# Kernel tuning notes

Measured on AMD Instinct MI355X. Metric: run time of the kernel, lower is better.

Reference implementation:

```python
import jax, jax.numpy as jnp
import numpy as np

N, E, H = 50000, 800000, 4

def setup_inputs() -> dict:
    key = jax.random.key(0)
    ks = jax.random.split(key, 16)
    feat = jax.random.normal(ks[0], (N, 2), dtype=jnp.float32)
    src = jax.random.randint(ks[1], (E,), 0, N, dtype=jnp.int32)
    dst = jax.random.randint(ks[2], (E,), 0, N, dtype=jnp.int32)
    def w(k, shape, fan_in):
        return jax.random.normal(k, shape, dtype=jnp.float32) * (1.0 / np.sqrt(fan_in))
    # layer 1: 2 -> 4 heads x 32
    W1 = w(ks[3], (2, 128), 2); al1 = w(ks[4], (H, 32), 32); ar1 = w(ks[5], (H, 32), 32); b1 = jnp.zeros((128,), jnp.float32)
    # layer 2: 128 -> 4 heads x 32
    W2 = w(ks[6], (128, 128), 128); al2 = w(ks[7], (H, 32), 32); ar2 = w(ks[8], (H, 32), 32); b2 = jnp.zeros((128,), jnp.float32)
    # layer 3: 128 -> 4 heads x 64
    W3 = w(ks[9], (128, 256), 128); al3 = w(ks[10], (H, 64), 64); ar3 = w(ks[11], (H, 64), 64); b3 = jnp.zeros((256,), jnp.float32)
    return dict(feat=feat, src=src, dst=dst, W1=W1, al1=al1, ar1=ar1, b1=b1,
                W2=W2, al2=al2, ar2=ar2, b2=b2, W3=W3, al3=al3, ar3=ar3, b3=b3)

def gat_layer(h, W, al, ar, b, src, dst):
    # h: [N, Fin]; W: [Fin, H*D]; al/ar: [H, D]; b: [H*D]
    Hh, D = al.shape
    z = (h @ W).reshape(-1, Hh, D)                      # [N, H, D]
    el = jnp.sum(z * al[None], axis=-1)                 # [N, H]
    er = jnp.sum(z * ar[None], axis=-1)                 # [N, H]
    e = jax.nn.leaky_relu(el[src] + er[dst], 0.2)       # [E, H]
    m = jax.ops.segment_max(e, dst, num_segments=N)     # [N, H] per-dst max
    ex = jnp.exp(e - m[dst])                            # [E, H]
    s = jax.ops.segment_sum(ex, dst, num_segments=N)    # [N, H]
    alpha = ex / s[dst]                                 # edge softmax
    msg = z[src] * alpha[:, :, None]                    # [E, H, D] gathered+weighted
    out = jax.ops.segment_sum(msg, dst, num_segments=N) # [N, H, D]
    return out.reshape(N, Hh * D) + b

def reference(feat, src, dst, W1, al1, ar1, b1, W2, al2, ar2, b2, W3, al3, ar3, b3):
    # dropout is identity at inference
    h = jax.nn.relu(gat_layer(feat, W1, al1, ar1, b1, src, dst))
    h = jax.nn.relu(gat_layer(h, W2, al2, ar2, b2, src, dst))
    h = gat_layer(h, W3, al3, ar3, b3, src, dst)
    return h
```

## Files before the change

### kernel.cpp

```cpp
#include <hip/hip_runtime.h>
#include <math.h>


#define NEG_BIG (-1e38f)

typedef _Float16 h8 __attribute__((ext_vector_type(8)));
typedef _Float16 h4 __attribute__((ext_vector_type(4)));

static inline int cdiv(int a, int b) { return (a + b - 1) / b; }

__device__ __forceinline__ float lrelu(float x) { return (x >= 0.f) ? x : 0.2f * x; }


__global__ void count_deg_kernel(const int* __restrict__ dst, int* __restrict__ deg, int E) {
    int i = blockIdx.x * blockDim.x + threadIdx.x;
    if (i < E) atomicAdd(&deg[dst[i]], 1);
}

__global__ __launch_bounds__(256) void scan1_kernel(const int* __restrict__ deg,
                                                    int* __restrict__ rowptr,
                                                    int* __restrict__ bsum, int n) {
    __shared__ int wsum[4];
    int t = threadIdx.x;
    int l = t & 63, wv = t >> 6;
    int i = blockIdx.x * 256 + t;
    int v = (i < n) ? deg[i] : 0;
    int x = v;
    #pragma unroll
    for (int off = 1; off < 64; off <<= 1) {
        int y = __shfl_up(x, off);
        if (l >= off) x += y;
    }
    if (l == 63) wsum[wv] = x;
    __syncthreads();
    int wo = 0;
    #pragma unroll
    for (int j = 0; j < 4; ++j)
        if (j < wv) wo += wsum[j];
    if (i < n) rowptr[i] = wo + x - v;
    if (t == 255) bsum[blockIdx.x] = wo + x;
}

__global__ __launch_bounds__(256) void scan2_kernel(const int* __restrict__ bsum,
                                                    int* __restrict__ boff, int nb) {
    __shared__ int wsum[4];
    int t = threadIdx.x;
    int l = t & 63, wv = t >> 6;
    int v = (t < nb) ? bsum[t] : 0;
    int x = v;
    #pragma unroll
    for (int off = 1; off < 64; off <<= 1) {
        int y = __shfl_up(x, off);
        if (l >= off) x += y;
    }
    if (l == 63) wsum[wv] = x;
    __syncthreads();
    int wo = 0;
    #pragma unroll
    for (int j = 0; j < 4; ++j)
        if (j < wv) wo += wsum[j];
    if (t < nb) boff[t] = wo + x - v;
}

__global__ __launch_bounds__(256) void scan3_kernel(int* __restrict__ rowptr,
                                                    const int* __restrict__ boff,
                                                    int n, int E) {
    int i = blockIdx.x * 256 + threadIdx.x;
    if (i < n) rowptr[i] += boff[blockIdx.x];
    if (i == 0) rowptr[n] = E;
}

__global__ void fill_csr_kernel(const int* __restrict__ src, const int* __restrict__ dst,
                                const int* __restrict__ rowptr,
                                int* __restrict__ cursor, int* __restrict__ csrc, int E) {
    int i = blockIdx.x * blockDim.x + threadIdx.x;
    if (i < E) {
        int d = dst[i];
        int pos = atomicAdd(&cursor[d], 1);
        csrc[rowptr[d] + pos] = src[i];
    }
}


__global__ void z1_kernel(const float* __restrict__ feat, const float* __restrict__ W1,
                          const float* __restrict__ al, const float* __restrict__ ar,
                          _Float16* __restrict__ zh, float* __restrict__ el,
                          float* __restrict__ er, int N) {
    int l = threadIdx.x & 63;
    int v = blockIdx.x * 4 + (threadIdx.x >> 6);
    if (v >= N) return;
    float f0 = feat[(size_t)v * 2];
    float f1 = feat[(size_t)v * 2 + 1];
    float z0 = fmaf(f0, W1[l], f1 * W1[128 + l]);
    float z1v = fmaf(f0, W1[l + 64], f1 * W1[128 + l + 64]);
    zh[(size_t)v * 128 + l] = (_Float16)z0;
    zh[(size_t)v * 128 + l + 64] = (_Float16)z1v;
    float pl0 = z0 * al[l], pl1 = z1v * al[l + 64];
    float pr0 = z0 * ar[l], pr1 = z1v * ar[l + 64];
    #pragma unroll
    for (int off = 1; off < 32; off <<= 1) {
        pl0 += __shfl_xor(pl0, off);
        pl1 += __shfl_xor(pl1, off);
        pr0 += __shfl_xor(pr0, off);
        pr1 += __shfl_xor(pr1, off);
    }
    if ((l & 31) == 0) {
        int g = l >> 5;
        el[(size_t)v * 4 + g] = pl0;
        el[(size_t)v * 4 + 2 + g] = pl1;
        er[(size_t)v * 4 + g] = pr0;
        er[(size_t)v * 4 + 2 + g] = pr1;
    }
}


template <int HDOUT>
__global__ __launch_bounds__(256) void gemm_tile_kernel(
        const _Float16* __restrict__ A, const float* __restrict__ W,
        const float* __restrict__ al, const float* __restrict__ ar,
        _Float16* __restrict__ ZH, float* __restrict__ el, float* __restrict__ er,
        int N) {
    __shared__ __align__(16) float AT[64][132];
    __shared__ __align__(16) float WS[64][64];
    int n0 = blockIdx.x * 128;
    int c0 = blockIdx.y * 64;
    int t = threadIdx.x;
    int tr = t >> 4;
    int tc = t & 15;

    float acc[8][4] = {};

    for (int kc = 0; kc < 128; kc += 64) {
        {
            int kk = (t & 7) * 8;
            int rb = t >> 3;
            #pragma unroll
            for (int it = 0; it < 4; ++it) {
                int r = rb + 32 * it;
                int n = n0 + r;
                h8 a;
                #pragma unroll
                for (int j = 0; j < 8; ++j) a[j] = (_Float16)0.f;
                if (n < N) a = *(const h8*)&A[(size_t)n * 128 + kc + kk];
                #pragma unroll
                for (int j = 0; j < 8; ++j) AT[kk + j][r] = (float)a[j];
            }
        }
        {
            int cc = (t & 15) * 4;
            int kb = t >> 4;
            #pragma unroll
            for (int it = 0; it < 4; ++it) {
                int k = kb + 16 * it;
                *(float4*)&WS[k][cc] =
                    *(const float4*)&W[(size_t)(kc + k) * HDOUT + c0 + cc];
            }
        }
        __syncthreads();

        #pragma unroll 4
        for (int k = 0; k < 64; ++k) {
            float4 a0 = *(const float4*)&AT[k][tr * 8];
            float4 a1 = *(const float4*)&AT[k][tr * 8 + 4];
            float4 wv = *(const float4*)&WS[k][tc * 4];
            acc[0][0] = fmaf(a0.x, wv.x, acc[0][0]); acc[0][1] = fmaf(a0.x, wv.y, acc[0][1]);
            acc[0][2] = fmaf(a0.x, wv.z, acc[0][2]); acc[0][3] = fmaf(a0.x, wv.w, acc[0][3]);
            acc[1][0] = fmaf(a0.y, wv.x, acc[1][0]); acc[1][1] = fmaf(a0.y, wv.y, acc[1][1]);
            acc[1][2] = fmaf(a0.y, wv.z, acc[1][2]); acc[1][3] = fmaf(a0.y, wv.w, acc[1][3]);
            acc[2][0] = fmaf(a0.z, wv.x, acc[2][0]); acc[2][1] = fmaf(a0.z, wv.y, acc[2][1]);
            acc[2][2] = fmaf(a0.z, wv.z, acc[2][2]); acc[2][3] = fmaf(a0.z, wv.w, acc[2][3]);
            acc[3][0] = fmaf(a0.w, wv.x, acc[3][0]); acc[3][1] = fmaf(a0.w, wv.y, acc[3][1]);
            acc[3][2] = fmaf(a0.w, wv.z, acc[3][2]); acc[3][3] = fmaf(a0.w, wv.w, acc[3][3]);
            acc[4][0] = fmaf(a1.x, wv.x, acc[4][0]); acc[4][1] = fmaf(a1.x, wv.y, acc[4][1]);
            acc[4][2] = fmaf(a1.x, wv.z, acc[4][2]); acc[4][3] = fmaf(a1.x, wv.w, acc[4][3]);
            acc[5][0] = fmaf(a1.y, wv.x, acc[5][0]); acc[5][1] = fmaf(a1.y, wv.y, acc[5][1]);
            acc[5][2] = fmaf(a1.y, wv.z, acc[5][2]); acc[5][3] = fmaf(a1.y, wv.w, acc[5][3]);
            acc[6][0] = fmaf(a1.z, wv.x, acc[6][0]); acc[6][1] = fmaf(a1.z, wv.y, acc[6][1]);
            acc[6][2] = fmaf(a1.z, wv.z, acc[6][2]); acc[6][3] = fmaf(a1.z, wv.w, acc[6][3]);
            acc[7][0] = fmaf(a1.w, wv.x, acc[7][0]); acc[7][1] = fmaf(a1.w, wv.y, acc[7][1]);
            acc[7][2] = fmaf(a1.w, wv.z, acc[7][2]); acc[7][3] = fmaf(a1.w, wv.w, acc[7][3]);
        }
        __syncthreads();
    }

    float4 alv = *(const float4*)&al[c0 + tc * 4];
    float4 arv = *(const float4*)&ar[c0 + tc * 4];

    #pragma unroll
    for (int i = 0; i < 8; ++i) {
        int n = n0 + tr * 8 + i;
        bool ok = (n < N);
        if (ok) {
            h4 hz4 = { (_Float16)acc[i][0], (_Float16)acc[i][1],
                       (_Float16)acc[i][2], (_Float16)acc[i][3] };
            *(h4*)&ZH[(size_t)n * HDOUT + c0 + tc * 4] = hz4;
        }
        float pe = acc[i][0] * alv.x + acc[i][1] * alv.y +
                   acc[i][2] * alv.z + acc[i][3] * alv.w;
        float pr = acc[i][0] * arv.x + acc[i][1] * arv.y +
                   acc[i][2] * arv.z + acc[i][3] * arv.w;
        if (HDOUT == 128) {
            #pragma unroll
            for (int off = 1; off < 8; off <<= 1) {
                pe += __shfl_xor(pe, off);
                pr += __shfl_xor(pr, off);
            }
            if (ok && (tc & 7) == 0) {
                int h = 2 * blockIdx.y + (tc >> 3);
                el[(size_t)n * 4 + h] = pe;
                er[(size_t)n * 4 + h] = pr;
            }
        } else {
            #pragma unroll
            for (int off = 1; off < 16; off <<= 1) {
                pe += __shfl_xor(pe, off);
                pr += __shfl_xor(pr, off);
            }
            if (ok && tc == 0) {
                int h = blockIdx.y;
                el[(size_t)n * 4 + h] = pe;
                er[(size_t)n * 4 + h] = pr;
            }
        }
    }
}


template <bool RELU, int GRP, int HD, typename OUTT>
__global__ __launch_bounds__(256) void agg_kernel(
        const _Float16* __restrict__ zh, const float* __restrict__ el,
        const float* __restrict__ er, const int* __restrict__ rowptr,
        const int* __restrict__ csrc, const float* __restrict__ bias,
        OUTT* __restrict__ out, int N) {
    constexpr int NV = 64 / GRP;
    constexpr int CH = HD / GRP;
    constexpr int HGRP = GRP / 4;
    static_assert(CH == 8, "config assumes 8 channels per lane");
    __shared__ float exs[4][NV][4][GRP + 1];
    __shared__ int   svs[4][NV][GRP + 1];
    const int l = threadIdx.x & 63;
    const int w = threadIdx.x >> 6;
    const int g = l / GRP;
    const int lg = l & (GRP - 1);
    const int v = blockIdx.x * (4 * NV) + w * NV + g;
    if (v >= N) return;
    const int r0 = rowptr[v], r1 = rowptr[v + 1];
    const int c0 = lg * CH;
    const int h = lg / HGRP;
    float4 b0 = *(const float4*)(bias + c0);
    float4 b1 = *(const float4*)(bias + c0 + 4);
    float4 o0, o1;

    if (r0 == r1) {
        o0 = b0; o1 = b1;
    } else {
        float4 er4 = *(const float4*)(er + (size_t)v * 4);

        float m0 = NEG_BIG, m1 = NEG_BIG, m2 = NEG_BIG, m3 = NEG_BIG;
        int sv0 = 0;
        float4 e40 = make_float4(NEG_BIG, NEG_BIG, NEG_BIG, NEG_BIG);
        for (int base = r0; base < r1; base += GRP) {
            int i = base + lg;
            float ex_ = NEG_BIG, ey_ = NEG_BIG, ez_ = NEG_BIG, ew_ = NEG_BIG;
            int sv = 0;
            if (i < r1) {
                sv = csrc[i];
                float4 ev = *(const float4*)(el + (size_t)sv * 4);
                ex_ = lrelu(ev.x + er4.x);
                ey_ = lrelu(ev.y + er4.y);
                ez_ = lrelu(ev.z + er4.z);
                ew_ = lrelu(ev.w + er4.w);
            }
            if (base == r0) { sv0 = sv; e40 = make_float4(ex_, ey_, ez_, ew_); }
            m0 = fmaxf(m0, ex_); m1 = fmaxf(m1, ey_);
            m2 = fmaxf(m2, ez_); m3 = fmaxf(m3, ew_);
        }
        #pragma unroll
        for (int off = 1; off < GRP; off <<= 1) {
            m0 = fmaxf(m0, __shfl_xor(m0, off));
            m1 = fmaxf(m1, __shfl_xor(m1, off));
            m2 = fmaxf(m2, __shfl_xor(m2, off));
            m3 = fmaxf(m3, __shfl_xor(m3, off));
        }

        float s0 = 0.f, s1 = 0.f, s2 = 0.f, s3 = 0.f;
        float4 a0 = make_float4(0.f, 0.f, 0.f, 0.f);
        float4 a1 = make_float4(0.f, 0.f, 0.f, 0.f);

        for (int base = r0; base < r1; base += GRP) {
            int i = base + lg;
            int sv; float4 e4;
            if (base == r0) {
                sv = sv0; e4 = e40;
            } else if (i < r1) {
                sv = csrc[i];
                float4 ev = *(const float4*)(el + (size_t)sv * 4);
                e4 = make_float4(lrelu(ev.x + er4.x), lrelu(ev.y + er4.y),
                                 lrelu(ev.z + er4.z), lrelu(ev.w + er4.w));
            } else {
                sv = 0; e4 = make_float4(NEG_BIG, NEG_BIG, NEG_BIG, NEG_BIG);
            }
            bool valid = (i < r1);
            float exv0 = valid ? __expf(e4.x - m0) : 0.f;
            float exv1 = valid ? __expf(e4.y - m1) : 0.f;
            float exv2 = valid ? __expf(e4.z - m2) : 0.f;
            float exv3 = valid ? __expf(e4.w - m3) : 0.f;
            s0 += exv0; s1 += exv1; s2 += exv2; s3 += exv3;
            svs[w][g][lg] = sv;
            exs[w][g][0][lg] = exv0; exs[w][g][1][lg] = exv1;
            exs[w][g][2][lg] = exv2; exs[w][g][3][lg] = exv3;
            int cnt = min(GRP, r1 - base);
            #pragma unroll 8
            for (int k = 0; k < cnt; ++k) {
                int svk = svs[w][g][k];
                float exk = exs[w][g][h][k];
                h8 zz = *(const h8*)(zh + (size_t)svk * HD + c0);
                a0.x = fmaf((float)zz[0], exk, a0.x);
                a0.y = fmaf((float)zz[1], exk, a0.y);
                a0.z = fmaf((float)zz[2], exk, a0.z);
                a0.w = fmaf((float)zz[3], exk, a0.w);
                a1.x = fmaf((float)zz[4], exk, a1.x);
                a1.y = fmaf((float)zz[5], exk, a1.y);
                a1.z = fmaf((float)zz[6], exk, a1.z);
                a1.w = fmaf((float)zz[7], exk, a1.w);
            }
        }
        #pragma unroll
        for (int off = 1; off < GRP; off <<= 1) {
            s0 += __shfl_xor(s0, off);
            s1 += __shfl_xor(s1, off);
            s2 += __shfl_xor(s2, off);
            s3 += __shfl_xor(s3, off);
        }
        float s = (h == 0) ? s0 : (h == 1) ? s1 : (h == 2) ? s2 : s3;
        float inv = 1.f / s;
        o0 = make_float4(fmaf(a0.x, inv, b0.x), fmaf(a0.y, inv, b0.y),
                         fmaf(a0.z, inv, b0.z), fmaf(a0.w, inv, b0.w));
        o1 = make_float4(fmaf(a1.x, inv, b1.x), fmaf(a1.y, inv, b1.y),
                         fmaf(a1.z, inv, b1.z), fmaf(a1.w, inv, b1.w));
    }
    if (RELU) {
        o0.x = fmaxf(o0.x, 0.f); o0.y = fmaxf(o0.y, 0.f);
        o0.z = fmaxf(o0.z, 0.f); o0.w = fmaxf(o0.w, 0.f);
        o1.x = fmaxf(o1.x, 0.f); o1.y = fmaxf(o1.y, 0.f);
        o1.z = fmaxf(o1.z, 0.f); o1.w = fmaxf(o1.w, 0.f);
    }
    if constexpr (sizeof(OUTT) == 2) {
        h8 ho;
        ho[0] = (_Float16)o0.x; ho[1] = (_Float16)o0.y;
        ho[2] = (_Float16)o0.z; ho[3] = (_Float16)o0.w;
        ho[4] = (_Float16)o1.x; ho[5] = (_Float16)o1.y;
        ho[6] = (_Float16)o1.z; ho[7] = (_Float16)o1.w;
        *(h8*)((_Float16*)out + (size_t)v * HD + c0) = ho;
    } else {
        float* op = (float*)out + (size_t)v * HD + c0;
        *(float4*)op = o0;
        *(float4*)(op + 4) = o1;
    }
}


extern "C" void kernel_launch(void* const* d_in, const int* in_sizes, int n_in,
                              void* d_out, int out_size, void* d_ws, size_t ws_size,
                              hipStream_t stream) {
    const float* feat = (const float*)d_in[0];
    const int* src = (const int*)d_in[1];
    const int* dst = (const int*)d_in[2];
    const float* W1 = (const float*)d_in[3];
    const float* al1 = (const float*)d_in[4];
    const float* ar1 = (const float*)d_in[5];
    const float* b1 = (const float*)d_in[6];
    const float* W2 = (const float*)d_in[7];
    const float* al2 = (const float*)d_in[8];
    const float* ar2 = (const float*)d_in[9];
    const float* b2 = (const float*)d_in[10];
    const float* W3 = (const float*)d_in[11];
    const float* al3 = (const float*)d_in[12];
    const float* ar3 = (const float*)d_in[13];
    const float* b3 = (const float*)d_in[14];
    const int N = in_sizes[0] / 2;
    const int E = in_sizes[1];

    _Float16* hbuf = (_Float16*)d_ws;
    float* el = (float*)(hbuf + (size_t)N * 128);
    float* er = el + (size_t)N * 4;
    _Float16* zh = (_Float16*)(er + (size_t)N * 4);
    int* csrc = (int*)(zh + (size_t)N * 256);
    int* deg = csrc + E;
    int* cursor = deg + N;
    int* rowptr = cursor + N;
    int* bsum = rowptr + (N + 1);
    int* boff = bsum + 256;

    const int nb = cdiv(N, 256);

    hipMemsetAsync(deg, 0, sizeof(int) * (size_t)(2 * N), stream);
    count_deg_kernel<<<cdiv(E, 256), 256, 0, stream>>>(dst, deg, E);
    scan1_kernel<<<nb, 256, 0, stream>>>(deg, rowptr, bsum, N);
    scan2_kernel<<<1, 256, 0, stream>>>(bsum, boff, nb);
    scan3_kernel<<<nb, 256, 0, stream>>>(rowptr, boff, N, E);
    fill_csr_kernel<<<cdiv(E, 256), 256, 0, stream>>>(src, dst, rowptr, cursor, csrc, E);

    const int nodeBlocks = cdiv(N, 4);

    z1_kernel<<<nodeBlocks, 256, 0, stream>>>(feat, W1, al1, ar1, zh, el, er, N);
    agg_kernel<true, 16, 128, _Float16><<<cdiv(N, 16), 256, 0, stream>>>(
        zh, el, er, rowptr, csrc, b1, hbuf, N);

    gemm_tile_kernel<128><<<dim3(cdiv(N, 128), 2), 256, 0, stream>>>(
        hbuf, W2, al2, ar2, zh, el, er, N);
    agg_kernel<true, 16, 128, _Float16><<<cdiv(N, 16), 256, 0, stream>>>(
        zh, el, er, rowptr, csrc, b2, hbuf, N);

    gemm_tile_kernel<256><<<dim3(cdiv(N, 128), 4), 256, 0, stream>>>(
        hbuf, W3, al3, ar3, zh, el, er, N);
    agg_kernel<false, 32, 256, float><<<cdiv(N, 8), 256, 0, stream>>>(
        zh, el, er, rowptr, csrc, b3, (float*)d_out, N);
}
```

Before: 353.6 us.

## Fuse layer-1 projection into aggregation using rank-2 input features

Replaces the layer-1 z computation kernel plus generic aggregation with one fused kernel. Because the input has only 2 features, the attention logits are computed from folded W1·al and W1·ar coefficients, and aggregation sums exp-weighted raw 2-d features before multiplying by W1. This avoids writing and gathering a 128-wide fp16 z tensor per edge and drops a kernel launch. In exchange it recomputes edge logits in two passes and adds shared-memory staging, and layer 1 now accumulates in fp32 rather than from fp16 z.

```diff
diff --git a/kernel.cpp b/kernel.cpp
--- a/kernel.cpp
+++ b/kernel.cpp
@@ -82,35 +82,163 @@
 }
 
 
-__global__ void z1_kernel(const float* __restrict__ feat, const float* __restrict__ W1,
-                          const float* __restrict__ al, const float* __restrict__ ar,
-                          _Float16* __restrict__ zh, float* __restrict__ el,
-                          float* __restrict__ er, int N) {
-    int l = threadIdx.x & 63;
-    int v = blockIdx.x * 4 + (threadIdx.x >> 6);
-    if (v >= N) return;
-    float f0 = feat[(size_t)v * 2];
-    float f1 = feat[(size_t)v * 2 + 1];
-    float z0 = fmaf(f0, W1[l], f1 * W1[128 + l]);
-    float z1v = fmaf(f0, W1[l + 64], f1 * W1[128 + l + 64]);
-    zh[(size_t)v * 128 + l] = (_Float16)z0;
-    zh[(size_t)v * 128 + l + 64] = (_Float16)z1v;
-    float pl0 = z0 * al[l], pl1 = z1v * al[l + 64];
-    float pr0 = z0 * ar[l], pr1 = z1v * ar[l + 64];
+__global__ __launch_bounds__(256) void agg1_kernel(
+        const float* __restrict__ feat, const float* __restrict__ W1,
+        const float* __restrict__ al, const float* __restrict__ ar,
+        const int* __restrict__ rowptr, const int* __restrict__ csrc,
+        const float* __restrict__ bias, _Float16* __restrict__ out, int N) {
+    constexpr int GRP = 16, NV = 4;
+    __shared__ float2 fss[4][NV][GRP + 1];
+    __shared__ float  exs[4][NV][4][GRP + 1];
+    const int l = threadIdx.x & 63;
+    const int w = threadIdx.x >> 6;
+    const int g = l >> 4;
+    const int lg = l & 15;
+    const int v = blockIdx.x * (4 * NV) + w * NV + g;
+
+    float w0l = W1[l], w0h = W1[l + 64];
+    float w1l = W1[128 + l], w1h = W1[128 + l + 64];
+    float all_ = al[l], alh = al[l + 64];
+    float arl = ar[l], arh = ar[l + 64];
+    float pa0 = w0l * all_, pa1 = w0h * alh;
+    float pb0 = w1l * all_, pb1 = w1h * alh;
+    float pc0 = w0l * arl,  pc1 = w0h * arh;
+    float pd0 = w1l * arl,  pd1 = w1h * arh;
     #pragma unroll
     for (int off = 1; off < 32; off <<= 1) {
-        pl0 += __shfl_xor(pl0, off);
-        pl1 += __shfl_xor(pl1, off);
-        pr0 += __shfl_xor(pr0, off);
-        pr1 += __shfl_xor(pr1, off);
-    }
-    if ((l & 31) == 0) {
-        int g = l >> 5;
-        el[(size_t)v * 4 + g] = pl0;
-        el[(size_t)v * 4 + 2 + g] = pl1;
-        er[(size_t)v * 4 + g] = pr0;
-        er[(size_t)v * 4 + 2 + g] = pr1;
-    }
+        pa0 += __shfl_xor(pa0, off); pa1 += __shfl_xor(pa1, off);
+        pb0 += __shfl_xor(pb0, off); pb1 += __shfl_xor(pb1, off);
+        pc0 += __shfl_xor(pc0, off); pc1 += __shfl_xor(pc1, off);
+        pd0 += __shfl_xor(pd0, off); pd1 += __shfl_xor(pd1, off);
+    }
+    float4 Ael = make_float4(__shfl(pa0, 0), __shfl(pa0, 32),
+                             __shfl(pa1, 0), __shfl(pa1, 32));
+    float4 Bel = make_float4(__shfl(pb0, 0), __shfl(pb0, 32),
+                             __shfl(pb1, 0), __shfl(pb1, 32));
+    float4 Aer = make_float4(__shfl(pc0, 0), __shfl(pc0, 32),
+                             __shfl(pc1, 0), __shfl(pc1, 32));
+    float4 Ber = make_float4(__shfl(pd0, 0), __shfl(pd0, 32),
+                             __shfl(pd1, 0), __shfl(pd1, 32));
+
+    if (v >= N) return;
+    const int r0 = rowptr[v], r1 = rowptr[v + 1];
+    const int c0 = lg * 8;
+    const int h = lg >> 2;
+    float4 w0a = *(const float4*)&W1[c0];
+    float4 w0b = *(const float4*)&W1[c0 + 4];
+    float4 w1a = *(const float4*)&W1[128 + c0];
+    float4 w1b = *(const float4*)&W1[128 + c0 + 4];
+    float4 b0 = *(const float4*)(bias + c0);
+    float4 b1 = *(const float4*)(bias + c0 + 4);
+    float4 o0, o1;
+
+    if (r0 == r1) {
+        o0 = b0; o1 = b1;
+    } else {
+        float2 fv = *(const float2*)(feat + (size_t)v * 2);
+        float4 er4 = make_float4(fmaf(fv.x, Aer.x, fv.y * Ber.x),
+                                 fmaf(fv.x, Aer.y, fv.y * Ber.y),
+                                 fmaf(fv.x, Aer.z, fv.y * Ber.z),
+                                 fmaf(fv.x, Aer.w, fv.y * Ber.w));
+
+        float m0 = NEG_BIG, m1 = NEG_BIG, m2 = NEG_BIG, m3 = NEG_BIG;
+        float2 fs0 = make_float2(0.f, 0.f);
+        float4 e40 = make_float4(NEG_BIG, NEG_BIG, NEG_BIG, NEG_BIG);
+        for (int base = r0; base < r1; base += GRP) {
+            int i = base + lg;
+            float ex_ = NEG_BIG, ey_ = NEG_BIG, ez_ = NEG_BIG, ew_ = NEG_BIG;
+            float2 fs = make_float2(0.f, 0.f);
+            if (i < r1) {
+                int sv = csrc[i];
+                fs = *(const float2*)(feat + (size_t)sv * 2);
+                ex_ = lrelu(fmaf(fs.x, Ael.x, fs.y * Bel.x) + er4.x);
+                ey_ = lrelu(fmaf(fs.x, Ael.y, fs.y * Bel.y) + er4.y);
+                ez_ = lrelu(fmaf(fs.x, Ael.z, fs.y * Bel.z) + er4.z);
+                ew_ = lrelu(fmaf(fs.x, Ael.w, fs.y * Bel.w) + er4.w);
+            }
+            if (base == r0) { fs0 = fs; e40 = make_float4(ex_, ey_, ez_, ew_); }
+            m0 = fmaxf(m0, ex_); m1 = fmaxf(m1, ey_);
+            m2 = fmaxf(m2, ez_); m3 = fmaxf(m3, ew_);
+        }
+        #pragma unroll
+        for (int off = 1; off < GRP; off <<= 1) {
+            m0 = fmaxf(m0, __shfl_xor(m0, off));
+            m1 = fmaxf(m1, __shfl_xor(m1, off));
+            m2 = fmaxf(m2, __shfl_xor(m2, off));
+            m3 = fmaxf(m3, __shfl_xor(m3, off));
+        }
+
+        float s0 = 0.f, s1 = 0.f, s2 = 0.f, s3 = 0.f;
+        float4 a0 = make_float4(0.f, 0.f, 0.f, 0.f);
+        float4 a1 = make_float4(0.f, 0.f, 0.f, 0.f);
+
+        for (int base = r0; base < r1; base += GRP) {
+            int i = base + lg;
+            float2 fs; float4 e4;
+            if (base == r0) {
+                fs = fs0; e4 = e40;
+            } else if (i < r1) {
+                int sv = csrc[i];
+                fs = *(const float2*)(feat + (size_t)sv * 2);
+                e4 = make_float4(
+                    lrelu(fmaf(fs.x, Ael.x, fs.y * Bel.x) + er4.x),
+                    lrelu(fmaf(fs.x, Ael.y, fs.y * Bel.y) + er4.y),
+                    lrelu(fmaf(fs.x, Ael.z, fs.y * Bel.z) + er4.z),
+                    lrelu(fmaf(fs.x, Ael.w, fs.y * Bel.w) + er4.w));
+            } else {
+                fs = make_float2(0.f, 0.f);
+                e4 = make_float4(NEG_BIG, NEG_BIG, NEG_BIG, NEG_BIG);
+            }
+            bool valid = (i < r1);
+            float exv0 = valid ? __expf(e4.x - m0) : 0.f;
+            float exv1 = valid ? __expf(e4.y - m1) : 0.f;
+            float exv2 = valid ? __expf(e4.z - m2) : 0.f;
+            float exv3 = valid ? __expf(e4.w - m3) : 0.f;
+            s0 += exv0; s1 += exv1; s2 += exv2; s3 += exv3;
+            fss[w][g][lg] = fs;
+            exs[w][g][0][lg] = exv0; exs[w][g][1][lg] = exv1;
+            exs[w][g][2][lg] = exv2; exs[w][g][3][lg] = exv3;
+            int cnt = min(GRP, r1 - base);
+            #pragma unroll 8
+            for (int k = 0; k < cnt; ++k) {
+                float2 fk = fss[w][g][k];
+                float exk = exs[w][g][h][k];
+                float u = fk.x * exk;
+                float t = fk.y * exk;
+                a0.x = fmaf(u, w0a.x, fmaf(t, w1a.x, a0.x));
+                a0.y = fmaf(u, w0a.y, fmaf(t, w1a.y, a0.y));
+                a0.z = fmaf(u, w0a.z, fmaf(t, w1a.z, a0.z));
+                a0.w = fmaf(u, w0a.w, fmaf(t, w1a.w, a0.w));
+                a1.x = fmaf(u, w0b.x, fmaf(t, w1b.x, a1.x));
+                a1.y = fmaf(u, w0b.y, fmaf(t, w1b.y, a1.y));
+                a1.z = fmaf(u, w0b.z, fmaf(t, w1b.z, a1.z));
+                a1.w = fmaf(u, w0b.w, fmaf(t, w1b.w, a1.w));
+            }
+        }
+        #pragma unroll
+        for (int off = 1; off < GRP; off <<= 1) {
+            s0 += __shfl_xor(s0, off);
+            s1 += __shfl_xor(s1, off);
+            s2 += __shfl_xor(s2, off);
+            s3 += __shfl_xor(s3, off);
+        }
+        float s = (h == 0) ? s0 : (h == 1) ? s1 : (h == 2) ? s2 : s3;
+        float inv = 1.f / s;
+        o0 = make_float4(fmaf(a0.x, inv, b0.x), fmaf(a0.y, inv, b0.y),
+                         fmaf(a0.z, inv, b0.z), fmaf(a0.w, inv, b0.w));
+        o1 = make_float4(fmaf(a1.x, inv, b1.x), fmaf(a1.y, inv, b1.y),
+                         fmaf(a1.z, inv, b1.z), fmaf(a1.w, inv, b1.w));
+    }
+    o0.x = fmaxf(o0.x, 0.f); o0.y = fmaxf(o0.y, 0.f);
+    o0.z = fmaxf(o0.z, 0.f); o0.w = fmaxf(o0.w, 0.f);
+    o1.x = fmaxf(o1.x, 0.f); o1.y = fmaxf(o1.y, 0.f);
+    o1.z = fmaxf(o1.z, 0.f); o1.w = fmaxf(o1.w, 0.f);
+    h8 ho;
+    ho[0] = (_Float16)o0.x; ho[1] = (_Float16)o0.y;
+    ho[2] = (_Float16)o0.z; ho[3] = (_Float16)o0.w;
+    ho[4] = (_Float16)o1.x; ho[5] = (_Float16)o1.y;
+    ho[6] = (_Float16)o1.z; ho[7] = (_Float16)o1.w;
+    *(h8*)(out + (size_t)v * 128 + c0) = ho;
 }
 
 
@@ -401,11 +529,8 @@
     scan3_kernel<<<nb, 256, 0, stream>>>(rowptr, boff, N, E);
     fill_csr_kernel<<<cdiv(E, 256), 256, 0, stream>>>(src, dst, rowptr, cursor, csrc, E);
 
-    const int nodeBlocks = cdiv(N, 4);
-
-    z1_kernel<<<nodeBlocks, 256, 0, stream>>>(feat, W1, al1, ar1, zh, el, er, N);
-    agg_kernel<true, 16, 128, _Float16><<<cdiv(N, 16), 256, 0, stream>>>(
-        zh, el, er, rowptr, csrc, b1, hbuf, N);
+    agg1_kernel<<<cdiv(N, 16), 256, 0, stream>>>(feat, W1, al1, ar1, rowptr, csrc,
+                                                 b1, hbuf, N);
 
     gemm_tile_kernel<128><<<dim3(cdiv(N, 128), 2), 256, 0, stream>>>(
         hbuf, W2, al2, ar2, zh, el, er, N);
```

Result: faster. 327.4 us (-7.4%).
